# Performance work log

Hardware: AMD Instinct MI355X
Metric: run time of the kernel (lower is better)

## Reference

```python
import jax, jax.numpy as jnp
import numpy as np

B, N_IN, UNITS = 512, 2048, 4096
DT = 1.0; GL = 30.0; CAP = 281.0; EL = -70.6; THR = -50.4; DELTAT = 2.0
TAUW = 144.0; A_W = 4.0; B_W = 0.0805; V_RESET = -70.6; N_REFRAC = 2; DAMP = 0.3
DT_GL_C = DT * GL / CAP
DT_A_TAUW = DT * A_W / TAUW

@jax.custom_vjp
def spike_function(v_scaled, dampening_factor):
    return (v_scaled > 0.0).astype(jnp.float32)

def _spike_fwd(v_scaled, dampening_factor):
    return spike_function(v_scaled, dampening_factor), (v_scaled, dampening_factor)

def _spike_bwd(res, g):
    v_scaled, damp = res
    # pseudo-derivative: damp * max(1 - |v_scaled|, 0)
    return (g * damp * jnp.maximum(1.0 - jnp.abs(v_scaled), 0.0), jnp.zeros_like(damp))

spike_function.defvjp(_spike_fwd, _spike_bwd)

def setup_inputs() -> dict:
    key = jax.random.key(0)
    ks = jax.random.split(key, 7)
    inputs = jax.random.normal(ks[0], (B, N_IN), jnp.float32)
    v = EL + 5.0 * jax.random.normal(ks[1], (B, UNITS), jnp.float32)  # membrane voltage near rest
    r = jax.random.randint(ks[2], (B, UNITS), 0, 3, jnp.int32)        # refractory counters
    w = jax.random.normal(ks[3], (B, UNITS), jnp.float32)             # adaptation current
    z = (jax.random.uniform(ks[4], (B, UNITS), jnp.float32) < 0.1).astype(jnp.float32)  # prev spikes
    input_weights = jax.random.uniform(ks[5], (N_IN, UNITS), jnp.float32, 0.0, 1.2)
    recurrent_weights = 0.7 * jax.random.normal(ks[6], (UNITS, UNITS), jnp.float32) / np.sqrt(UNITS)
    return {"inputs": inputs, "v": v, "r": r, "w": w, "z": z,
            "input_weights": input_weights, "recurrent_weights": recurrent_weights}

def reference(inputs, v, r, w, z, input_weights, recurrent_weights):
    # mask autapses (diagonal) and enforce sign constraint (Dale's law)
    diag = jnp.eye(UNITS, dtype=bool)
    no_autapse = jnp.where(diag, 0.0, recurrent_weights)
    rec_sign = jnp.sign(recurrent_weights)
    constrained_w_rec = jnp.where(rec_sign * no_autapse >= 0.0, no_autapse, 0.0)
    # input + recurrent currents
    i_t = inputs @ input_weights + z @ constrained_w_rec  # [B, UNITS]
    # AdEx exponential term (clipped, gradient stopped)
    exp_terms = jax.lax.stop_gradient(
        jnp.clip(jnp.exp((v - THR) / DELTAT), -1.0e6, 30.0 / DT_GL_C))
    new_v = v - DT_GL_C * (v - EL) + DT_GL_C * DELTAT * exp_terms + (i_t - w) * DT / CAP
    new_v = jnp.where(z > 0.5, jnp.float32(V_RESET), new_v)  # reset after spike
    new_w = w - DT / TAUW * w + DT_A_TAUW * (v - EL) + B_W * z
    v_scaled = -(THR - new_v) / (THR - EL)
    new_z = spike_function(v_scaled, jnp.float32(DAMP))
    new_z = jnp.where(r > 0, 0.0, new_z)  # refractory neurons cannot spike
    new_r = jnp.clip(r - 1 + (new_z * N_REFRAC).astype(jnp.int32), 0, N_REFRAC)
    return (new_v, new_z, new_w, new_r)
```

## Files before the change

kernel.cpp:

```cpp
#include <hip/hip_runtime.h>
#include <stdint.h>

#define B_SZ   512
#define NIN    2048
#define UNITS  4096
#define KTOT   (NIN + UNITS)
#define BM     32
#define BN     128
#define BK     32
#define BSTR   36

typedef __attribute__((ext_vector_type(8))) __bf16        bf16x8;
typedef __attribute__((ext_vector_type(4))) float         f32x4;

__device__ __forceinline__ unsigned int fbits(float f) {
    unsigned int u; __builtin_memcpy(&u, &f, 4); return u;
}
__device__ __forceinline__ float tof(unsigned int u) {
    float f; __builtin_memcpy(&f, &u, 4); return f;
}

__device__ __forceinline__ void lds_barrier() {
    asm volatile("s_waitcnt lgkmcnt(0)\n\ts_barrier" ::: "memory");
}

__device__ __forceinline__ void adex_one(float it, float v, float w, float z, int r,
                                         float& nv, float& nz, float& nw, float& nr)
{
    const float EL = -70.6f, THR = -50.4f;
    const float dt_gl_c    = (float)(30.0 / 281.0);
    const float dt_gl_c_dt = (float)(60.0 / 281.0);
    const float dt_tauw    = (float)(1.0 / 144.0);
    const float dt_a_tauw  = (float)(4.0 / 144.0);
    float ex = expf((v - THR) * 0.5f);
    ex = fminf(ex, 281.0f);
    float vv = v - dt_gl_c * (v - EL) + dt_gl_c_dt * ex + (it - w) / 281.0f;
    if (z > 0.5f) vv = -70.6f;
    nv = vv;
    nw = w - dt_tauw * w + dt_a_tauw * (v - EL) + 0.0805f * z;
    float s = (vv > THR) ? 1.0f : 0.0f;
    if (r > 0) s = 0.0f;
    nz = s;
    int ri = r - 1 + (s > 0.5f ? 2 : 0);
    ri = ri < 0 ? 0 : (ri > 2 ? 2 : ri);
    nr = (float)ri;
}

__global__ __launch_bounds__(256, 2)
void adex_fused(const float* __restrict__ inp,
                const float* __restrict__ zsp,
                const float* __restrict__ Win,
                const float* __restrict__ Wrec,
                const float* __restrict__ v_in,
                const float* __restrict__ w_in,
                const int*   __restrict__ r_in,
                float*       __restrict__ out)
{
    __shared__ unsigned short Ah[BM * BK];
    __shared__ unsigned short Al[BM * BK];
    __shared__ unsigned short Bh[BN * BSTR];
    __shared__ unsigned short Bl[BN * BSTR];

    const int tid = threadIdx.x;
    const int l   = tid & 63;
    const int w   = tid >> 6;
    const int lm  = l & 15;
    const int q   = l >> 4;
    const int bn0 = blockIdx.x * BN;
    const int bm0 = blockIdx.y * BM;
    const int wm  = (w >> 1) * 16;
    const int wn  = (w & 1) * 64;

    const int ar = tid >> 3;
    const int kq = tid & 7;
    const int bkk = 2 * (tid & 15);
    const int bnn = 8 * (tid >> 4);

    const float* pAin = inp + (size_t)(bm0 + ar) * NIN   + kq * 4;
    const float* pAz  = zsp + (size_t)(bm0 + ar) * UNITS + kq * 4;
    const float* pBin = Win  + (size_t)bkk * UNITS + bn0 + bnn;
    const float* pBrc = Wrec + (size_t)bkk * UNITS + bn0 + bnn;

    f32x4 acc[4];
    const f32x4 zero4 = {0.f, 0.f, 0.f, 0.f};
    #pragma unroll
    for (int j = 0; j < 4; ++j) acc[j] = zero4;

    float4 aS0 = *(const float4*)(pAin);
    float4 aS1 = *(const float4*)(pAin + 32);
    float4 s0b0a = *(const float4*)(pBin);
    float4 s0b0b = *(const float4*)(pBin + 4);
    float4 s0b1a = *(const float4*)(pBin + UNITS);
    float4 s0b1b = *(const float4*)(pBin + UNITS + 4);
    const float* pB32 = pBin + (size_t)32 * UNITS;
    float4 s1b0a = *(const float4*)(pB32);
    float4 s1b0b = *(const float4*)(pB32 + 4);
    float4 s1b1a = *(const float4*)(pB32 + UNITS);
    float4 s1b1b = *(const float4*)(pB32 + UNITS + 4);

    auto tile = [&](float4& aT, float4& c0a, float4& c0b, float4& c1a, float4& c1b,
                    int k0) {
        const bool full = (k0 < NIN);

        {
            const unsigned int u0 = fbits(aT.x), u1 = fbits(aT.y),
                               u2 = fbits(aT.z), u3 = fbits(aT.w);
            uint2 H = { (u0 >> 16) | (u1 & 0xffff0000u),
                        (u2 >> 16) | (u3 & 0xffff0000u) };
            *(uint2*)(Ah + ar * BK + kq * 4) = H;
            if (full) {
                const float h0 = tof(u0 & 0xffff0000u), h1 = tof(u1 & 0xffff0000u);
                const float h2 = tof(u2 & 0xffff0000u), h3 = tof(u3 & 0xffff0000u);
                const unsigned int l0 = fbits(aT.x - h0), l1 = fbits(aT.y - h1);
                const unsigned int l2 = fbits(aT.z - h2), l3 = fbits(aT.w - h3);
                uint2 L = { (l0 >> 16) | (l1 & 0xffff0000u),
                            (l2 >> 16) | (l3 & 0xffff0000u) };
                *(uint2*)(Al + ar * BK + kq * 4) = L;
            }
        }
        {
            const float r0[8] = {c0a.x, c0a.y, c0a.z, c0a.w, c0b.x, c0b.y, c0b.z, c0b.w};
            const float r1[8] = {c1a.x, c1a.y, c1a.z, c1a.w, c1b.x, c1b.y, c1b.z, c1b.w};
            #pragma unroll
            for (int c = 0; c < 8; ++c) {
                const unsigned int u_0 = fbits(r0[c]), u_1 = fbits(r1[c]);
                *(unsigned int*)(Bh + (bnn + c) * BSTR + bkk) =
                    (u_0 >> 16) | (u_1 & 0xffff0000u);
                const float h0 = tof(u_0 & 0xffff0000u), h1 = tof(u_1 & 0xffff0000u);
                const unsigned int l_0 = fbits(r0[c] - h0), l_1 = fbits(r1[c] - h1);
                *(unsigned int*)(Bl + (bnn + c) * BSTR + bkk) =
                    (l_0 >> 16) | (l_1 & 0xffff0000u);
            }
        }
        lds_barrier();

        const int kp = k0 + 64;
        if (kp < KTOT) {
            aT = *(const float4*)((kp < NIN) ? pAin + kp : pAz + (kp - NIN));
            const float* bp = (kp < NIN) ? pBin + (size_t)kp * UNITS
                                         : pBrc + (size_t)(kp - NIN) * UNITS;
            c0a = *(const float4*)(bp);
            c0b = *(const float4*)(bp + 4);
            c1a = *(const float4*)(bp + UNITS);
            c1b = *(const float4*)(bp + UNITS + 4);
        }

        bf16x8 ah_, al_ = {};
        {
            const int off = (wm + lm) * BK + q * 8;
            ah_ = *(const bf16x8*)(Ah + off);
            if (full) al_ = *(const bf16x8*)(Al + off);
        }
        bf16x8 bh_[4], bl_[4];
        #pragma unroll
        for (int j = 0; j < 4; ++j) {
            const int off = (wn + j * 16 + lm) * BSTR + q * 8;
            const uint2 ha = *(const uint2*)(Bh + off);
            const uint2 hb = *(const uint2*)(Bh + off + 4);
            const uint2 la = *(const uint2*)(Bl + off);
            const uint2 lb = *(const uint2*)(Bl + off + 4);
            uint4 hu = { ha.x, ha.y, hb.x, hb.y };
            uint4 lu = { la.x, la.y, lb.x, lb.y };
            bh_[j] = __builtin_bit_cast(bf16x8, hu);
            bl_[j] = __builtin_bit_cast(bf16x8, lu);
        }
        #pragma unroll
        for (int j = 0; j < 4; ++j) {
            acc[j] = __builtin_amdgcn_mfma_f32_16x16x32_bf16(ah_, bh_[j], acc[j], 0, 0, 0);
            acc[j] = __builtin_amdgcn_mfma_f32_16x16x32_bf16(ah_, bl_[j], acc[j], 0, 0, 0);
        }
        if (full) {
            #pragma unroll
            for (int j = 0; j < 4; ++j)
                acc[j] = __builtin_amdgcn_mfma_f32_16x16x32_bf16(al_, bh_[j], acc[j], 0, 0, 0);
        }

        lds_barrier();
    };

    #pragma unroll 1
    for (int k0 = 0; k0 < KTOT; k0 += 64) {
        tile(aS0, s0b0a, s0b0b, s0b1a, s0b1b, k0);
        tile(aS1, s1b0a, s1b0b, s1b1a, s1b1b, k0 + 32);
    }

    const size_t CH = (size_t)B_SZ * UNITS;
    float dgv[4];
    #pragma unroll
    for (int j = 0; j < 4; ++j) {
        const int n = bn0 + wn + j * 16 + lm;
        dgv[j] = Wrec[(size_t)n * UNITS + n];
    }
    #pragma unroll
    for (int rr = 0; rr < 4; ++rr) {
        const int b = bm0 + wm + q * 4 + rr;
        const size_t rowb = (size_t)b * UNITS;
        #pragma unroll
        for (int j = 0; j < 4; ++j) {
            const int n = bn0 + wn + j * 16 + lm;
            const size_t idx = rowb + n;
            const float vv = v_in[idx];
            const float wv = w_in[idx];
            const float zv = zsp[idx];
            const int   rv = r_in[idx];
            const float it = acc[j][rr] - zv * dgv[j];
            float nv, nz, nw, nr;
            adex_one(it, vv, wv, zv, rv, nv, nz, nw, nr);
            out[idx]          = nv;
            out[CH + idx]     = nz;
            out[2 * CH + idx] = nw;
            out[3 * CH + idx] = nr;
        }
    }
}

extern "C" void kernel_launch(void* const* d_in, const int* in_sizes, int n_in,
                              void* d_out, int out_size, void* d_ws, size_t ws_size,
                              hipStream_t stream) {
    (void)in_sizes; (void)n_in; (void)out_size; (void)d_ws; (void)ws_size;
    const float* inp  = (const float*)d_in[0];
    const float* v    = (const float*)d_in[1];
    const int*   r    = (const int*)d_in[2];
    const float* w    = (const float*)d_in[3];
    const float* z    = (const float*)d_in[4];
    const float* Win  = (const float*)d_in[5];
    const float* Wrec = (const float*)d_in[6];
    float* out = (float*)d_out;

    dim3 g(UNITS / BN, B_SZ / BM);
    adex_fused<<<g, dim3(256), 0, stream>>>(inp, z, Win, Wrec, v, w, r, out);
}
```

Before: 364.4 us.

## Pre-split operands into swizzled bf16 hi/lo workspace and stream via LDS-direct loads

Adds two prep kernels that convert the activations and weights into bf16 hi/lo pairs laid out in k-tile-major, XOR-swizzled workspace buffers. The recurrent diagonal is zeroed during prep rather than subtracted afterwards. A new GEMM kernel double-buffers those tiles into LDS with global_load_lds, so the per-tile float-to-bf16 splitting and transposition are removed from the main loop. The cost is an extra full pass over both weight matrices to write the roughly 100 MB workspace, plus two additional launches. The original fused kernel remains as a fallback when no workspace is available.

After: 317.3 us. 1.15x faster.

```diff
diff --git a/kernel.cpp b/kernel.cpp
--- a/kernel.cpp
+++ b/kernel.cpp
@@ -5,6 +5,10 @@
 #define NIN    2048
 #define UNITS  4096
 #define KTOT   (NIN + UNITS)
+#define KT_N   (KTOT / 32)
+#define KT_WIN (NIN / 32)
+#define GBM    32
+#define GBN    128
 #define BM     32
 #define BN     128
 #define BK     32
@@ -13,11 +17,23 @@
 typedef __attribute__((ext_vector_type(8))) __bf16        bf16x8;
 typedef __attribute__((ext_vector_type(4))) float         f32x4;
 
+typedef const void __attribute__((address_space(1)))* gas1_t;
+typedef void       __attribute__((address_space(3)))* las3_t;
+
 __device__ __forceinline__ unsigned int fbits(float f) {
     unsigned int u; __builtin_memcpy(&u, &f, 4); return u;
 }
 __device__ __forceinline__ float tof(unsigned int u) {
     float f; __builtin_memcpy(&f, &u, 4); return f;
+}
+
+__device__ __forceinline__ void gload16(const void* g, void* l) {
+    __builtin_amdgcn_global_load_lds((gas1_t)g, (las3_t)l, 16, 0, 0);
+}
+
+__device__ __forceinline__ void pipe_barrier() {
+    __builtin_amdgcn_s_barrier();
+    asm volatile("" ::: "memory");
 }
 
 __device__ __forceinline__ void lds_barrier() {
@@ -46,6 +62,211 @@
     nr = (float)ri;
 }
 
+
+__global__ __launch_bounds__(256)
+void prep_A(const float* __restrict__ inp, const float* __restrict__ zsp,
+            unsigned short* __restrict__ Ap)
+{
+    const int kt    = blockIdx.y;
+    const int mb    = blockIdx.x;
+    const int t     = threadIdx.x;
+    const int m_loc = t >> 3;
+    const int c     = t & 7;
+    const int q     = c & 3;
+    const int m     = mb * 32 + m_loc;
+
+    const float* src = (kt < KT_WIN)
+        ? inp + (size_t)m * NIN   + kt * 32 + q * 8
+        : zsp + (size_t)m * UNITS + (kt - KT_WIN) * 32 + q * 8;
+    const float4 a = *(const float4*)(src);
+    const float4 b = *(const float4*)(src + 4);
+    const float x[8] = {a.x, a.y, a.z, a.w, b.x, b.y, b.z, b.w};
+
+    unsigned int wd[4];
+    if (c < 4) {
+        #pragma unroll
+        for (int i = 0; i < 4; ++i)
+            wd[i] = (fbits(x[2*i]) >> 16) | (fbits(x[2*i+1]) & 0xffff0000u);
+    } else {
+        #pragma unroll
+        for (int i = 0; i < 4; ++i) {
+            const float l0 = x[2*i]   - tof(fbits(x[2*i])   & 0xffff0000u);
+            const float l1 = x[2*i+1] - tof(fbits(x[2*i+1]) & 0xffff0000u);
+            wd[i] = (fbits(l0) >> 16) | (fbits(l1) & 0xffff0000u);
+        }
+    }
+    const uint4 v4 = {wd[0], wd[1], wd[2], wd[3]};
+    *(uint4*)(Ap + ((size_t)kt * B_SZ + m) * 64 + ((c ^ (m_loc & 7)) * 8)) = v4;
+}
+
+__global__ __launch_bounds__(256)
+void prep_B(const float* __restrict__ Win, const float* __restrict__ Wrec,
+            unsigned short* __restrict__ Bp)
+{
+    __shared__ float lt[32][65];
+    const int kt = blockIdx.y;
+    const int nt = blockIdx.x;
+    const int n0 = nt * 64;
+    const int t  = threadIdx.x;
+
+    {
+        const int kr = t >> 3, cc = (t & 7) * 8;
+        const float* src = ((kt < KT_WIN)
+            ? Win  + (size_t)(kt * 32 + kr) * UNITS
+            : Wrec + (size_t)((kt - KT_WIN) * 32 + kr) * UNITS) + n0 + cc;
+        const float4 a = *(const float4*)(src);
+        const float4 b = *(const float4*)(src + 4);
+        lt[kr][cc+0] = a.x; lt[kr][cc+1] = a.y; lt[kr][cc+2] = a.z; lt[kr][cc+3] = a.w;
+        lt[kr][cc+4] = b.x; lt[kr][cc+5] = b.y; lt[kr][cc+6] = b.z; lt[kr][cc+7] = b.w;
+    }
+    __syncthreads();
+
+    const int n_loc = t >> 2;
+    const int q     = t & 3;
+    const int n     = n0 + n_loc;
+    float x[8];
+    #pragma unroll
+    for (int j = 0; j < 8; ++j) x[j] = lt[q * 8 + j][n_loc];
+
+    if (kt >= KT_WIN) {
+        const int kg = (kt - KT_WIN) * 32 + q * 8;
+        #pragma unroll
+        for (int j = 0; j < 8; ++j) if (kg + j == n) x[j] = 0.f;
+    }
+
+    unsigned int hw[4], lw[4];
+    #pragma unroll
+    for (int i = 0; i < 4; ++i) {
+        hw[i] = (fbits(x[2*i]) >> 16) | (fbits(x[2*i+1]) & 0xffff0000u);
+        const float l0 = x[2*i]   - tof(fbits(x[2*i])   & 0xffff0000u);
+        const float l1 = x[2*i+1] - tof(fbits(x[2*i+1]) & 0xffff0000u);
+        lw[i] = (fbits(l0) >> 16) | (fbits(l1) & 0xffff0000u);
+    }
+    const int nkey = n_loc & 7;
+    unsigned short* base = Bp + ((size_t)kt * UNITS + n) * 64;
+    const uint4 hv = {hw[0], hw[1], hw[2], hw[3]};
+    const uint4 lv = {lw[0], lw[1], lw[2], lw[3]};
+    *(uint4*)(base + ((q       ^ nkey) * 8)) = hv;
+    *(uint4*)(base + (((4 + q) ^ nkey) * 8)) = lv;
+}
+
+__global__ __launch_bounds__(256, 2)
+void adex_gemm(const unsigned short* __restrict__ Ap,
+               const unsigned short* __restrict__ Bp,
+               const float* __restrict__ v_in,
+               const float* __restrict__ w_in,
+               const float* __restrict__ zsp,
+               const int*   __restrict__ r_in,
+               float*       __restrict__ out)
+{
+    __shared__ unsigned short Bl[2][GBN * 64];
+    __shared__ unsigned short Al[2][GBM * 64];
+
+    const int tid = threadIdx.x;
+    const int l   = tid & 63;
+    const int w   = tid >> 6;
+    const int lm  = l & 15;
+    const int q   = l >> 4;
+    const int bn0 = blockIdx.x * GBN;
+    const int bm0 = blockIdx.y * GBM;
+    const int wn  = w * 32;
+
+    const unsigned short* Abase = Ap + (size_t)bm0 * 64;
+    const unsigned short* Bbase = Bp + (size_t)bn0 * 64;
+
+    f32x4 acc[2][2];
+    const f32x4 zero4 = {0.f, 0.f, 0.f, 0.f};
+    #pragma unroll
+    for (int mr = 0; mr < 2; ++mr)
+        #pragma unroll
+        for (int nr = 0; nr < 2; ++nr) acc[mr][nr] = zero4;
+
+    auto stage = [&](int buf, int kt) {
+        const unsigned short* bs = Bbase + (size_t)kt * UNITS * 64;
+        #pragma unroll
+        for (int i = 0; i < 4; ++i)
+            gload16(bs + (size_t)(i * 256 + tid) * 8,
+                    &Bl[buf][(i * 256 + w * 64) * 8]);
+        const unsigned short* as = Abase + (size_t)kt * B_SZ * 64;
+        gload16(as + (size_t)tid * 8, &Al[buf][(w * 64) * 8]);
+    };
+
+    auto compute = [&](int buf, int kt) {
+        const bool full = (kt < KT_WIN);
+        bf16x8 ah[2], al2[2], bh[2], bl2[2];
+        #pragma unroll
+        for (int mr = 0; mr < 2; ++mr) {
+            const int ml = mr * 16 + lm;
+            const unsigned short* ab = &Al[buf][ml * 64];
+            ah[mr] = *(const bf16x8*)(ab + ((q ^ (ml & 7)) * 8));
+            if (full)
+                al2[mr] = *(const bf16x8*)(ab + (((4 + q) ^ (ml & 7)) * 8));
+        }
+        #pragma unroll
+        for (int nr = 0; nr < 2; ++nr) {
+            const int nl = wn + nr * 16 + lm;
+            const unsigned short* bb = &Bl[buf][nl * 64];
+            bh[nr]  = *(const bf16x8*)(bb + ((q ^ (nl & 7)) * 8));
+            bl2[nr] = *(const bf16x8*)(bb + (((4 + q) ^ (nl & 7)) * 8));
+        }
+        #pragma unroll
+        for (int mr = 0; mr < 2; ++mr)
+            #pragma unroll
+            for (int nr = 0; nr < 2; ++nr) {
+                acc[mr][nr] = __builtin_amdgcn_mfma_f32_16x16x32_bf16(ah[mr],  bh[nr],  acc[mr][nr], 0, 0, 0);
+                acc[mr][nr] = __builtin_amdgcn_mfma_f32_16x16x32_bf16(ah[mr],  bl2[nr], acc[mr][nr], 0, 0, 0);
+                if (full)
+                    acc[mr][nr] = __builtin_amdgcn_mfma_f32_16x16x32_bf16(al2[mr], bh[nr], acc[mr][nr], 0, 0, 0);
+            }
+    };
+
+    stage(0, 0);
+    #pragma unroll 1
+    for (int kt = 0; kt < KT_N; kt += 2) {
+        stage(1, kt + 1);
+        asm volatile("s_waitcnt vmcnt(5)" ::: "memory");
+        pipe_barrier();
+        compute(0, kt);
+        asm volatile("s_waitcnt lgkmcnt(0)" ::: "memory");
+        pipe_barrier();
+        if (kt + 2 < KT_N) {
+            stage(0, kt + 2);
+            asm volatile("s_waitcnt vmcnt(5)" ::: "memory");
+        } else {
+            asm volatile("s_waitcnt vmcnt(0)" ::: "memory");
+        }
+        pipe_barrier();
+        compute(1, kt + 1);
+        asm volatile("s_waitcnt lgkmcnt(0)" ::: "memory");
+        pipe_barrier();
+    }
+
+    const size_t CH = (size_t)B_SZ * UNITS;
+    #pragma unroll
+    for (int mr = 0; mr < 2; ++mr) {
+        #pragma unroll
+        for (int rr = 0; rr < 4; ++rr) {
+            const int b = bm0 + mr * 16 + q * 4 + rr;
+            const size_t rowb = (size_t)b * UNITS;
+            #pragma unroll
+            for (int nr = 0; nr < 2; ++nr) {
+                const int n = bn0 + wn + nr * 16 + lm;
+                const size_t idx = rowb + n;
+                const float vv = v_in[idx];
+                const float wv = w_in[idx];
+                const float zv = zsp[idx];
+                const int   rv = r_in[idx];
+                float nv, nz, nw, nr_;
+                adex_one(acc[mr][nr][rr], vv, wv, zv, rv, nv, nz, nw, nr_);
+                out[idx]          = nv;
+                out[CH + idx]     = nz;
+                out[2 * CH + idx] = nw;
+                out[3 * CH + idx] = nr_;
+            }
+        }
+    }
+}
+
 __global__ __launch_bounds__(256, 2)
 void adex_fused(const float* __restrict__ inp,
                 const float* __restrict__ zsp,
@@ -101,7 +322,6 @@
     auto tile = [&](float4& aT, float4& c0a, float4& c0b, float4& c1a, float4& c1b,
                     int k0) {
         const bool full = (k0 < NIN);
-
         {
             const unsigned int u0 = fbits(aT.x), u1 = fbits(aT.y),
                                u2 = fbits(aT.z), u3 = fbits(aT.w);
@@ -217,7 +437,7 @@
 extern "C" void kernel_launch(void* const* d_in, const int* in_sizes, int n_in,
                               void* d_out, int out_size, void* d_ws, size_t ws_size,
                               hipStream_t stream) {
-    (void)in_sizes; (void)n_in; (void)out_size; (void)d_ws; (void)ws_size;
+    (void)in_sizes; (void)n_in; (void)out_size;
     const float* inp  = (const float*)d_in[0];
     const float* v    = (const float*)d_in[1];
     const int*   r    = (const int*)d_in[2];
@@ -227,6 +447,18 @@
     const float* Wrec = (const float*)d_in[6];
     float* out = (float*)d_out;
 
-    dim3 g(UNITS / BN, B_SZ / BM);
-    adex_fused<<<g, dim3(256), 0, stream>>>(inp, z, Win, Wrec, v, w, r, out);
-}
+    const size_t A_BYTES = (size_t)KT_N * B_SZ  * 128;
+    const size_t B_BYTES = (size_t)KT_N * UNITS * 128;
+
+    if (d_ws != nullptr && ws_size >= A_BYTES + B_BYTES) {
+        unsigned short* Ap = (unsigned short*)d_ws;
+        unsigned short* Bp = (unsigned short*)((char*)d_ws + A_BYTES);
+        prep_A<<<dim3(16, KT_N), dim3(256), 0, stream>>>(inp, z, Ap);
+        prep_B<<<dim3(64, KT_N), dim3(256), 0, stream>>>(Win, Wrec, Bp);
+        adex_gemm<<<dim3(UNITS / GBN, B_SZ / GBM), dim3(256), 0, stream>>>(
+            Ap, Bp, v, w, z, r, out);
+    } else {
+        adex_fused<<<dim3(UNITS / BN, B_SZ / BM), dim3(256), 0, stream>>>(
+            inp, z, Win, Wrec, v, w, r, out);
+    }
+}
```
